# Kernel tuning notes

Measured on AMD Instinct MI355X. Metric: run time of the kernel, lower is better.

The kernel has to match this reference:

```python
import jax, jax.numpy as jnp
import numpy as np

K = 3      # kernel size (hardcoded 3x3 in the torch module via repeat(...,9,...))
PAD = 1
STRIDE = 1


def _unfold(x):
    # torch.nn.functional.unfold equivalent: (B,C,H,W) -> (B,C,K,K,oh,ow)
    B, C, H, W = x.shape
    p = jax.lax.conv_general_dilated_patches(
        x, (K, K), (STRIDE, STRIDE), ((PAD, PAD), (PAD, PAD)))
    oh, ow = p.shape[2], p.shape[3]
    return p.reshape(B, C, K, K, oh, ow)


def setup_inputs() -> dict:
    key = jax.random.key(0)
    k1, k2, k3, k4 = jax.random.split(key, 4)
    B, Cin, Cout, H, W = 4, 64, 64, 128, 128
    inputs = jax.random.normal(k1, (B, Cin, H, W), jnp.float32)
    depth = jax.random.uniform(k2, (B, 1, H, W), jnp.float32)  # positive depths
    weight = jax.random.uniform(k3, (K, Cout, Cin, K, K), jnp.float32, minval=-0.05, maxval=0.05)
    bias = jax.random.uniform(k4, (Cout,), jnp.float32, minval=-0.05, maxval=0.05)
    return {"inputs": inputs, "depth": depth, "weight": weight, "bias": bias, "f": 1}


def reference(inputs, depth, weight, bias, f):
    # --- DepthKernelFn: per-depth-plane binary masks ---
    depth_wins = _unfold(depth)          # (B,1,K,K,oh,ow)
    s_wins = depth_wins / f              # grid spacing s_i = d / f
    cy, cx = K // 2, K // 2
    d0 = depth_wins[:, :, cy, cx]        # center depth      (B,1,oh,ow)
    s0 = s_wins[:, :, cy, cx]            # center spacing    (B,1,oh,ow)
    offs = jnp.arange(K, dtype=inputs.dtype) - (K - 1) / 2.0  # l - (K-1)/2
    # z_l at center: d0 + (l-1)*s0  -> (K,B,1,oh,ow)
    z0 = d0[None] + offs[:, None, None, None, None] * s0[None]
    half = s0[None] / 2
    a = (z0 - half)[:, :, :, None, None]  # (K,B,1,1,1,oh,ow)
    b = (z0 + half)[:, :, :, None, None]
    dw = depth_wins[None]                 # (1,B,1,K,K,oh,ow)
    # mask_l = 1 where a <= depth < b else 0  (same as the where-cascade in torch)
    mask = ((dw >= a) & (dw < b)).astype(inputs.dtype)  # (K,B,1,K,K,oh,ow)

    # --- RepeatKernelConvFn: masked windowed conv via einsum ---
    inp_wins = _unfold(inputs)            # (B,C,K,K,oh,ow)
    x = inp_wins[None] * mask             # (K,B,C,K,K,oh,ow), depth C=1 broadcasts
    out = jnp.einsum('hijklmn,hojkl->iomn', x, weight)
    out = out + bias.reshape(1, -1, 1, 1)
    return out
```

## Files before the change

kernel.cpp:

```cpp
#include <hip/hip_runtime.h>
#include <math.h>

#define B_N  4
#define CIN  64
#define COUT 64
#define H_N  128
#define W_N  128

typedef _Float16 half8 __attribute__((ext_vector_type(8)));
typedef float    f32x4 __attribute__((ext_vector_type(4)));

#define KTOT   1728
#define NSTEP  54
#define WA_BYTES ((size_t)NSTEP * 4 * 64 * 8 * 2)

__global__ void wprep(const float* __restrict__ w, _Float16* __restrict__ wa) {
    int idx = blockIdx.x * 256 + threadIdx.x;
    if (idx >= NSTEP * 4 * 64) return;
    int lane = idx & 63;
    int mt   = (idx >> 6) & 3;
    int s    = idx >> 8;
    int m    = mt * 16 + (lane & 15);
    int kl0  = (lane >> 4) * 8;
    _Float16 v[8];
#pragma unroll
    for (int j = 0; j < 8; ++j) {
        int k = s * 32 + kl0 + j;
        int g = k >> 6;
        int c = k & 63;
        int t = g / 3;
        int h = g % 3;
        v[j] = (_Float16)w[(((size_t)(h * COUT) + m) * CIN + c) * 9 + t];
    }
    *(int4*)&wa[(size_t)idx * 8] = *(int4*)v;
}

#define XS_LINE 64
#define XS_ROW  (66 * XS_LINE)

__global__ __launch_bounds__(256, 3)
void conv_mfma(const float* __restrict__ inp, const float* __restrict__ depth,
               const _Float16* __restrict__ wa, const float* __restrict__ bias,
               const int* __restrict__ fptr, float* __restrict__ out) {
    __shared__ _Float16 Xs[3 * XS_ROW];
    __shared__ unsigned hLds[64];

    int bid  = blockIdx.x;
    int xh   = bid & 1;
    int y    = (bid >> 1) & (H_N - 1);
    int b    = bid >> 8;
    int x0   = xh * 64;
    int tid  = threadIdx.x;
    int lane = tid & 63;
    int mq   = tid >> 6;
    int ln15 = lane & 15;
    int quad = lane >> 4;

    int xl   = tid & 63;
    int cq   = tid >> 6;
    int xi   = xl + 1;
    int key  = xi & 7;
    int side = (tid >> 3) & 1;
    int ck   = tid & 7;
    int xi2  = side ? 65 : 0;
    int xg   = x0 + xi2 - 1;
    int key2 = xi2 & 7;

    const size_t HW = (size_t)H_N * W_N;

#define LOAD_ROW(dyi, buf, hbuf) {                                            \
        int yy_ = y + (dyi) - 1;                                              \
        if (yy_ >= 0 && yy_ < H_N) {                                          \
            const float* src_ = inp + (((size_t)b * CIN + cq * 16) * H_N + yy_) * W_N + (x0 + xl); \
            _Pragma("unroll")                                                 \
            for (int cc = 0; cc < 16; ++cc) buf[cc] = src_[(size_t)cc * HW];  \
        } else {                                                              \
            _Pragma("unroll")                                                 \
            for (int cc = 0; cc < 16; ++cc) buf[cc] = 0.f;                    \
        }                                                                     \
        if (tid < 16) {                                                       \
            if (xg >= 0 && xg < W_N && yy_ >= 0 && yy_ < H_N) {               \
                const float* hsrc_ = inp + (((size_t)b * CIN + ck * 8) * H_N + yy_) * W_N + xg; \
                _Pragma("unroll")                                             \
                for (int cc = 0; cc < 8; ++cc) hbuf[cc] = hsrc_[(size_t)cc * HW]; \
            } else {                                                          \
                _Pragma("unroll")                                             \
                for (int cc = 0; cc < 8; ++cc) hbuf[cc] = 0.f;                \
            }                                                                 \
        }                                                                     \
    }

#define WRITE_ROW(dyi, buf, hbuf) {                                           \
        _Float16 hb_[16];                                                     \
        _Pragma("unroll")                                                     \
        for (int cc = 0; cc < 16; ++cc) hb_[cc] = (_Float16)buf[cc];          \
        _Float16* dst_ = &Xs[(dyi) * XS_ROW + xi * XS_LINE];                  \
        *(int4*)&dst_[((cq * 2    ) ^ key) * 8] = *(int4*)&hb_[0];            \
        *(int4*)&dst_[((cq * 2 + 1) ^ key) * 8] = *(int4*)&hb_[8];            \
        if (tid < 16) {                                                       \
            _Float16 hh_[8];                                                  \
            _Pragma("unroll")                                                 \
            for (int cc = 0; cc < 8; ++cc) hh_[cc] = (_Float16)hbuf[cc];      \
            *(int4*)&Xs[(dyi) * XS_ROW + xi2 * XS_LINE + (ck ^ key2) * 8] = *(int4*)&hh_[0]; \
        }                                                                     \
    }

    const half8* wa8 = (const half8*)wa;
    half8 Abuf[2][6];

    float rbuf[16];
    float rhbuf[8];
    LOAD_ROW(0, rbuf, rhbuf);

    {
        const half8* bA = wa8 + (size_t)mq * 64 + lane;
#pragma unroll
        for (int j = 0; j < 6; ++j) Abuf[0][j] = bA[(size_t)j * 4 * 64];
    }

    if (tid < 64) {
        int x = x0 + tid;
        double fd  = (double)(*fptr);
        float  d0f = depth[((size_t)b * H_N + y) * W_N + x];
        double dd  = (double)d0f;
        double inv = fd / dd;
        bool   pos = (inv > 0.0);
        unsigned pk = 0;
        for (int t = 0; t < 9; ++t) {
            int dy = t / 3 - 1, dx = t % 3 - 1;
            int yy = y + dy, xx = x + dx;
            float dwf = (yy >= 0 && yy < H_N && xx >= 0 && xx < W_N)
                        ? depth[((size_t)b * H_N + yy) * W_N + xx] : 0.f;
            int h = -1;
            if (pos) {
                double u  = ((double)dwf - dd) * inv + 1.5;
                double uf = floor(u);
                if (uf >= 0.0 && uf <= 2.0) h = (int)uf;
            }
            pk |= (unsigned)(h + 1) << (2 * t);
        }
        hLds[tid] = pk;
    }

    WRITE_ROW(0, rbuf, rhbuf);
    __syncthreads();

    unsigned hpk[4];
#pragma unroll
    for (int nt = 0; nt < 4; ++nt) hpk[nt] = hLds[nt * 16 + ln15];

    f32x4 acc[4];
#pragma unroll
    for (int nt = 0; nt < 4; ++nt) acc[nt] = (f32x4){0.f, 0.f, 0.f, 0.f};

    half8 z8 = {(_Float16)0.f, (_Float16)0.f, (_Float16)0.f, (_Float16)0.f,
                (_Float16)0.f, (_Float16)0.f, (_Float16)0.f, (_Float16)0.f};

#pragma unroll
    for (int r = 0; r < 3; ++r) {
        float nbuf[16];
        float nhbuf[8];
        if (r < 2) LOAD_ROW(r + 1, nbuf, nhbuf);

#pragma unroll
        for (int dxl = 0; dxl < 3; ++dxl) {
            int t  = r * 3 + dxl;
            int dx = dxl - 1;

            half8 bb[8];
#pragma unroll
            for (int nt = 0; nt < 4; ++nt) {
                int xs = nt * 16 + ln15 + dx + 1;
                int k2 = xs & 7;
                int ba = r * XS_ROW + xs * XS_LINE;
                bb[nt * 2 + 0] = *(const half8*)&Xs[ba + ((quad    ) ^ k2) * 8];
                bb[nt * 2 + 1] = *(const half8*)&Xs[ba + ((quad + 4) ^ k2) * 8];
            }

            if (t < 8) {
                const half8* bA = wa8 + ((size_t)(t + 1) * 24 + mq) * 64 + lane;
#pragma unroll
                for (int j = 0; j < 6; ++j) Abuf[(t + 1) & 1][j] = bA[(size_t)j * 4 * 64];
            }

            int hb[4];
#pragma unroll
            for (int nt = 0; nt < 4; ++nt) hb[nt] = (hpk[nt] >> (2 * t)) & 3;

#pragma unroll
            for (int h = 0; h < 3; ++h) {
#pragma unroll
                for (int kk = 0; kk < 2; ++kk) {
                    int j = h * 2 + kk;
#pragma unroll
                    for (int nt = 0; nt < 4; ++nt) {
                        half8 c = (hb[nt] == h + 1) ? bb[nt * 2 + kk] : z8;
                        acc[nt] = __builtin_amdgcn_mfma_f32_16x16x32_f16(Abuf[t & 1][j], c, acc[nt], 0, 0, 0);
                    }
                }
            }
        }

        if (r < 2) {
            WRITE_ROW(r + 1, nbuf, nhbuf);
            __syncthreads();
        }
    }
#undef LOAD_ROW
#undef WRITE_ROW

#pragma unroll
    for (int nt = 0; nt < 4; ++nt) {
        int x = x0 + nt * 16 + ln15;
#pragma unroll
        for (int rr = 0; rr < 4; ++rr) {
            int o = mq * 16 + quad * 4 + rr;
            out[(((size_t)b * COUT + o) * H_N + y) * W_N + x] = acc[nt][rr] + bias[o];
        }
    }
}

__global__ __launch_bounds__(256)
void conv25d(const float* __restrict__ inp, const float* __restrict__ depth,
             const float* __restrict__ wsrc, const float* __restrict__ bias,
             const int* __restrict__ fptr, float* __restrict__ out) {
    int bid = blockIdx.x;
    int xt  = bid & 3;
    int y   = (bid >> 2) & (H_N - 1);
    int b   = bid >> 9;
    int o   = threadIdx.x & 63;
    int q   = threadIdx.x >> 6;
    int x0  = xt * 32 + q * 8;
    double fd = (double)(*fptr);
    float acc[8];
    float bv = bias[o];
#pragma unroll
    for (int i = 0; i < 8; ++i) acc[i] = bv;
    const float* dcen = depth + ((size_t)b * H_N + y) * W_N;
    float d0[8];
#pragma unroll
    for (int i = 0; i < 8; ++i) d0[i] = dcen[x0 + i];
    for (int t = 0; t < 9; ++t) {
        int dy = t / 3 - 1, dx = t % 3 - 1;
        int yy = y + dy;
        if (yy < 0 || yy >= H_N) continue;
        const float* drow = depth + ((size_t)b * H_N + yy) * W_N;
        int hsel[8];
#pragma unroll
        for (int i = 0; i < 8; ++i) {
            int xx = x0 + i + dx;
            int h = -1;
            if (xx >= 0 && xx < W_N) {
                double dd = (double)d0[i];
                double s0 = dd / fd;
                if (s0 > 0.0) {
                    double u = ((double)drow[xx] - dd) / s0 + 1.5;
                    double uf = floor(u);
                    if (uf >= 0.0 && uf <= 2.0) h = (int)uf;
                }
            }
            hsel[i] = h;
        }
        const float* irow = inp + ((size_t)b * CIN * H_N + yy) * W_N;
        for (int c = 0; c < CIN; ++c) {
            const float* wb = wsrc + ((size_t)o * CIN + c) * 9 + t;
            float w0 = wb[0], w1 = wb[(size_t)COUT * CIN * 9], w2 = wb[2 * (size_t)COUT * CIN * 9];
            const float* ir = irow + (size_t)c * H_N * W_N;
#pragma unroll
            for (int i = 0; i < 8; ++i) {
                int h = hsel[i];
                if (h >= 0) {
                    float wv = (h == 0) ? w0 : ((h == 1) ? w1 : w2);
                    acc[i] = fmaf(ir[x0 + i + dx], wv, acc[i]);
                }
            }
        }
    }
    float* orow = out + (((size_t)b * COUT + o) * H_N + y) * W_N;
#pragma unroll
    for (int i = 0; i < 8; ++i) orow[x0 + i] = acc[i];
}

extern "C" void kernel_launch(void* const* d_in, const int* in_sizes, int n_in,
                              void* d_out, int out_size, void* d_ws, size_t ws_size,
                              hipStream_t stream) {
    const float* inp   = (const float*)d_in[0];
    const float* depth = (const float*)d_in[1];
    const float* w     = (const float*)d_in[2];
    const float* bias  = (const float*)d_in[3];
    const int*   f     = (const int*)d_in[4];
    float* out = (float*)d_out;

    if (ws_size >= WA_BYTES) {
        _Float16* wa = (_Float16*)d_ws;
        wprep<<<NSTEP, 256, 0, stream>>>(w, wa);
        conv_mfma<<<B_N * H_N * 2, 256, 0, stream>>>(inp, depth, wa, bias, f, out);
    } else {
        conv25d<<<B_N * H_N * (W_N / 32), 256, 0, stream>>>(inp, depth, w, bias, f, out);
    }
}
```

Before: 99.50 us.

## Process full 128-pixel row per block to reuse weight fragments across twice the columns

Each block now covers a full output row (128 pixels) instead of half a row. Every weight fragment loaded from global memory is therefore reused over 8 column tiles instead of 4, and the halo loads are replaced by zero-padding the image borders in shared memory. The cost is twice the accumulators, B fragments and staging registers per thread, a larger shared-memory tile, occupancy lowered from 3 to 2 blocks per CU, and half as many blocks (512), which leaves less parallelism to hide latency.

```diff
diff --git a/kernel.cpp b/kernel.cpp
--- a/kernel.cpp
+++ b/kernel.cpp
@@ -36,81 +36,58 @@
 }
 
 #define XS_LINE 64
-#define XS_ROW  (66 * XS_LINE)
-
-__global__ __launch_bounds__(256, 3)
+#define XS_ROW  (130 * XS_LINE)
+
+__global__ __launch_bounds__(256, 2)
 void conv_mfma(const float* __restrict__ inp, const float* __restrict__ depth,
                const _Float16* __restrict__ wa, const float* __restrict__ bias,
                const int* __restrict__ fptr, float* __restrict__ out) {
     __shared__ _Float16 Xs[3 * XS_ROW];
-    __shared__ unsigned hLds[64];
+    __shared__ unsigned hLds[128];
 
     int bid  = blockIdx.x;
-    int xh   = bid & 1;
-    int y    = (bid >> 1) & (H_N - 1);
-    int b    = bid >> 8;
-    int x0   = xh * 64;
+    int y    = bid & (H_N - 1);
+    int b    = bid >> 7;
     int tid  = threadIdx.x;
     int lane = tid & 63;
     int mq   = tid >> 6;
     int ln15 = lane & 15;
     int quad = lane >> 4;
 
-    int xl   = tid & 63;
-    int cq   = tid >> 6;
-    int xi   = xl + 1;
-    int key  = xi & 7;
-    int side = (tid >> 3) & 1;
-    int ck   = tid & 7;
-    int xi2  = side ? 65 : 0;
-    int xg   = x0 + xi2 - 1;
-    int key2 = xi2 & 7;
+    int xl    = tid & 127;
+    int chalf = tid >> 7;
+    int xi    = xl + 1;
+    int key   = xi & 7;
 
     const size_t HW = (size_t)H_N * W_N;
 
-#define LOAD_ROW(dyi, buf, hbuf) {                                            \
+#define LOAD_ROW(dyi, buf) {                                                  \
         int yy_ = y + (dyi) - 1;                                              \
         if (yy_ >= 0 && yy_ < H_N) {                                          \
-            const float* src_ = inp + (((size_t)b * CIN + cq * 16) * H_N + yy_) * W_N + (x0 + xl); \
+            const float* src_ = inp + (((size_t)b * CIN + chalf * 32) * H_N + yy_) * W_N + xl; \
             _Pragma("unroll")                                                 \
-            for (int cc = 0; cc < 16; ++cc) buf[cc] = src_[(size_t)cc * HW];  \
+            for (int cc = 0; cc < 32; ++cc) buf[cc] = src_[(size_t)cc * HW];  \
         } else {                                                              \
             _Pragma("unroll")                                                 \
-            for (int cc = 0; cc < 16; ++cc) buf[cc] = 0.f;                    \
+            for (int cc = 0; cc < 32; ++cc) buf[cc] = 0.f;                    \
         }                                                                     \
-        if (tid < 16) {                                                       \
-            if (xg >= 0 && xg < W_N && yy_ >= 0 && yy_ < H_N) {               \
-                const float* hsrc_ = inp + (((size_t)b * CIN + ck * 8) * H_N + yy_) * W_N + xg; \
-                _Pragma("unroll")                                             \
-                for (int cc = 0; cc < 8; ++cc) hbuf[cc] = hsrc_[(size_t)cc * HW]; \
-            } else {                                                          \
-                _Pragma("unroll")                                             \
-                for (int cc = 0; cc < 8; ++cc) hbuf[cc] = 0.f;                \
-            }                                                                 \
-        }                                                                     \
-    }
-
-#define WRITE_ROW(dyi, buf, hbuf) {                                           \
-        _Float16 hb_[16];                                                     \
+    }
+
+#define WRITE_ROW(dyi, buf) {                                                 \
+        _Float16 hb_[32];                                                     \
         _Pragma("unroll")                                                     \
-        for (int cc = 0; cc < 16; ++cc) hb_[cc] = (_Float16)buf[cc];          \
+        for (int cc = 0; cc < 32; ++cc) hb_[cc] = (_Float16)buf[cc];          \
         _Float16* dst_ = &Xs[(dyi) * XS_ROW + xi * XS_LINE];                  \
-        *(int4*)&dst_[((cq * 2    ) ^ key) * 8] = *(int4*)&hb_[0];            \
-        *(int4*)&dst_[((cq * 2 + 1) ^ key) * 8] = *(int4*)&hb_[8];            \
-        if (tid < 16) {                                                       \
-            _Float16 hh_[8];                                                  \
-            _Pragma("unroll")                                                 \
-            for (int cc = 0; cc < 8; ++cc) hh_[cc] = (_Float16)hbuf[cc];      \
-            *(int4*)&Xs[(dyi) * XS_ROW + xi2 * XS_LINE + (ck ^ key2) * 8] = *(int4*)&hh_[0]; \
-        }                                                                     \
+        _Pragma("unroll")                                                     \
+        for (int k = 0; k < 4; ++k)                                           \
+            *(int4*)&dst_[((chalf * 4 + k) ^ key) * 8] = *(int4*)&hb_[k * 8]; \
     }
 
     const half8* wa8 = (const half8*)wa;
     half8 Abuf[2][6];
 
-    float rbuf[16];
-    float rhbuf[8];
-    LOAD_ROW(0, rbuf, rhbuf);
+    float rbuf[32];
+    LOAD_ROW(0, rbuf);
 
     {
         const half8* bA = wa8 + (size_t)mq * 64 + lane;
@@ -118,8 +95,17 @@
         for (int j = 0; j < 6; ++j) Abuf[0][j] = bA[(size_t)j * 4 * 64];
     }
 
-    if (tid < 64) {
-        int x = x0 + tid;
+    if (tid < 48) {
+        int dyi = tid / 16;
+        int rem = tid % 16;
+        int xz  = (rem >= 8) ? 129 : 0;
+        int k8  = rem & 7;
+        int4 z  = {0, 0, 0, 0};
+        *(int4*)&Xs[dyi * XS_ROW + xz * XS_LINE + k8 * 8] = z;
+    }
+
+    if (tid < 128) {
+        int x = tid;
         double fd  = (double)(*fptr);
         float  d0f = depth[((size_t)b * H_N + y) * W_N + x];
         double dd  = (double)d0f;
@@ -142,34 +128,33 @@
         hLds[tid] = pk;
     }
 
-    WRITE_ROW(0, rbuf, rhbuf);
+    WRITE_ROW(0, rbuf);
     __syncthreads();
 
-    unsigned hpk[4];
-#pragma unroll
-    for (int nt = 0; nt < 4; ++nt) hpk[nt] = hLds[nt * 16 + ln15];
-
-    f32x4 acc[4];
-#pragma unroll
-    for (int nt = 0; nt < 4; ++nt) acc[nt] = (f32x4){0.f, 0.f, 0.f, 0.f};
+    unsigned hpk[8];
+#pragma unroll
+    for (int nt = 0; nt < 8; ++nt) hpk[nt] = hLds[nt * 16 + ln15];
+
+    f32x4 acc[8];
+#pragma unroll
+    for (int nt = 0; nt < 8; ++nt) acc[nt] = (f32x4){0.f, 0.f, 0.f, 0.f};
 
     half8 z8 = {(_Float16)0.f, (_Float16)0.f, (_Float16)0.f, (_Float16)0.f,
                 (_Float16)0.f, (_Float16)0.f, (_Float16)0.f, (_Float16)0.f};
 
 #pragma unroll
     for (int r = 0; r < 3; ++r) {
-        float nbuf[16];
-        float nhbuf[8];
-        if (r < 2) LOAD_ROW(r + 1, nbuf, nhbuf);
+        float nbuf[32];
+        if (r < 2) LOAD_ROW(r + 1, nbuf);
 
 #pragma unroll
         for (int dxl = 0; dxl < 3; ++dxl) {
             int t  = r * 3 + dxl;
             int dx = dxl - 1;
 
-            half8 bb[8];
-#pragma unroll
-            for (int nt = 0; nt < 4; ++nt) {
+            half8 bb[16];
+#pragma unroll
+            for (int nt = 0; nt < 8; ++nt) {
                 int xs = nt * 16 + ln15 + dx + 1;
                 int k2 = xs & 7;
                 int ba = r * XS_ROW + xs * XS_LINE;
@@ -183,9 +168,9 @@
                 for (int j = 0; j < 6; ++j) Abuf[(t + 1) & 1][j] = bA[(size_t)j * 4 * 64];
             }
 
-            int hb[4];
-#pragma unroll
-            for (int nt = 0; nt < 4; ++nt) hb[nt] = (hpk[nt] >> (2 * t)) & 3;
+            int hb[8];
+#pragma unroll
+            for (int nt = 0; nt < 8; ++nt) hb[nt] = (hpk[nt] >> (2 * t)) & 3;
 
 #pragma unroll
             for (int h = 0; h < 3; ++h) {
@@ -193,7 +178,7 @@
                 for (int kk = 0; kk < 2; ++kk) {
                     int j = h * 2 + kk;
 #pragma unroll
-                    for (int nt = 0; nt < 4; ++nt) {
+                    for (int nt = 0; nt < 8; ++nt) {
                         half8 c = (hb[nt] == h + 1) ? bb[nt * 2 + kk] : z8;
                         acc[nt] = __builtin_amdgcn_mfma_f32_16x16x32_f16(Abuf[t & 1][j], c, acc[nt], 0, 0, 0);
                     }
@@ -202,7 +187,7 @@
         }
 
         if (r < 2) {
-            WRITE_ROW(r + 1, nbuf, nhbuf);
+            WRITE_ROW(r + 1, nbuf);
             __syncthreads();
         }
     }
@@ -210,8 +195,8 @@
 #undef WRITE_ROW
 
 #pragma unroll
-    for (int nt = 0; nt < 4; ++nt) {
-        int x = x0 + nt * 16 + ln15;
+    for (int nt = 0; nt < 8; ++nt) {
+        int x = nt * 16 + ln15;
 #pragma unroll
         for (int rr = 0; rr < 4; ++rr) {
             int o = mq * 16 + quad * 4 + rr;
@@ -294,7 +279,7 @@
     if (ws_size >= WA_BYTES) {
         _Float16* wa = (_Float16*)d_ws;
         wprep<<<NSTEP, 256, 0, stream>>>(w, wa);
-        conv_mfma<<<B_N * H_N * 2, 256, 0, stream>>>(inp, depth, wa, bias, f, out);
+        conv_mfma<<<B_N * H_N, 256, 0, stream>>>(inp, depth, wa, bias, f, out);
     } else {
         conv25d<<<B_N * H_N * (W_N / 32), 256, 0, stream>>>(inp, depth, w, bias, f, out);
     }
```

New measurement: 96.65 us, median of 2. -2.9%, faster.
